# Kernel tuning notes

Hardware: AMD Instinct MI355X
Metric: run time of the kernel (lower is better)

The kernel has to match this reference:

```python
import jax, jax.numpy as jnp
import numpy as np

BSZ, MAX_LEN, INPUT_DIM = 4, 256, 1024
BIAFFINE, OUT, N_HEAD = 512, 512, 4
IN_HD = BIAFFINE // N_HEAD   # 128
OUT_HD = OUT // N_HEAD       # 128


def setup_inputs() -> dict:
    key = jax.random.key(0)
    ks = jax.random.split(key, 6)
    x = jax.random.normal(ks[0], (BSZ, MAX_LEN, INPUT_DIM), dtype=jnp.float32)
    # head/tail MLP linear params (dropout is identity at inference)
    scale_lin = 1.0 / np.sqrt(INPUT_DIM)
    Wh = jax.random.normal(ks[1], (BIAFFINE, INPUT_DIM), dtype=jnp.float32) * scale_lin
    bh = jnp.zeros((BIAFFINE,), dtype=jnp.float32)
    Wv = jax.random.normal(ks[2], (BIAFFINE, INPUT_DIM), dtype=jnp.float32) * scale_lin
    bv = jnp.zeros((BIAFFINE,), dtype=jnp.float32)
    # biaffine tensor, xavier_normal over last two dims fan
    xav = np.sqrt(2.0 / (IN_HD + IN_HD))
    W = jax.random.normal(ks[3], (N_HEAD, OUT_HD, IN_HD, IN_HD), dtype=jnp.float32) * xav
    return {"x": x, "Wh": Wh, "bh": bh, "Wv": Wv, "bv": bv, "W": W}


def reference(x, Wh, bh, Wv, bv, W):
    # head/tail MLPs: Linear + LeakyReLU (slope 0.01, torch default)
    h = jax.nn.leaky_relu(jnp.einsum('bld,od->blo', x, Wh) + bh)  # b l biaffine
    v = jax.nn.leaky_relu(jnp.einsum('bld,od->blo', x, Wv) + bv)
    bsz, max_len, _ = h.shape
    h = h.reshape(bsz, max_len, N_HEAD, IN_HD)
    v = v.reshape(bsz, max_len, N_HEAD, IN_HD)
    # 3-way biaffine contraction
    w = jnp.einsum('blhx,hdxy,bkhy->bhdlk', h, W, v)  # b h out_hd l k
    w = w.reshape(bsz, OUT, max_len, max_len)
    return jnp.transpose(w, (0, 2, 3, 1))  # b l k out
```

## Files before the change

kernel.cpp:

```cpp
#include <hip/hip_runtime.h>


typedef unsigned short u16;
typedef __attribute__((ext_vector_type(8))) short short8;
typedef __attribute__((ext_vector_type(4))) float f32x4;

__device__ __forceinline__ u16 f2bf(float f) {
  union { float f; unsigned u; } c; c.f = f;
  unsigned u = c.u;
  return (u16)((u + 0x7FFFu + ((u >> 16) & 1u)) >> 16);
}

__device__ __forceinline__ unsigned pack2(float a, float b) {
  return ((unsigned)f2bf(b) << 16) | (unsigned)f2bf(a);
}

__device__ __forceinline__ uint4 pack8(const float* __restrict__ g) {
  float4 f0 = *(const float4*)(g);
  float4 f1 = *(const float4*)(g + 4);
  uint4 o;
  o.x = pack2(f0.x, f0.y);
  o.y = pack2(f0.z, f0.w);
  o.z = pack2(f1.x, f1.y);
  o.w = pack2(f1.z, f1.w);
  return o;
}

__device__ __forceinline__ void tile_compute(const u16* As, const u16* Bs,
                                             f32x4 acc[4][4], int wm, int wn,
                                             int frow, int kq) {
  short8 af[4], bfr[4];
#pragma unroll
  for (int i = 0; i < 4; ++i)
    af[i] = *(const short8*)(As + (size_t)(wm + i * 16 + frow) * 32 + kq);
#pragma unroll
  for (int j = 0; j < 4; ++j)
    bfr[j] = *(const short8*)(Bs + (size_t)(wn + j * 16 + frow) * 32 + kq);
#pragma unroll
  for (int i = 0; i < 4; ++i)
#pragma unroll
    for (int j = 0; j < 4; ++j)
      acc[i][j] = __builtin_amdgcn_mfma_f32_16x16x32_bf16(af[i], bfr[j], acc[i][j], 0, 0, 0);
}

__device__ __forceinline__ void stage_bf16(const u16* __restrict__ ga,
                                           const u16* __restrict__ gb,
                                           u16* As, u16* Bs, int r, int seg) {
  uint4 a0 = *(const uint4*)ga;
  uint4 a1 = *(const uint4*)(ga + 8);
  uint4 b0 = *(const uint4*)gb;
  uint4 b1 = *(const uint4*)(gb + 8);
  __syncthreads();
  *(uint4*)(As + r * 32 + seg * 16) = a0;
  *(uint4*)(As + r * 32 + seg * 16 + 8) = a1;
  *(uint4*)(Bs + r * 32 + seg * 16) = b0;
  *(uint4*)(Bs + r * 32 + seg * 16 + 8) = b1;
  __syncthreads();
}

__global__ __launch_bounds__(256) void k0_twp(const float* __restrict__ W,
                                              u16* __restrict__ Wb) {
  __shared__ u16 t[128][129];
  int slice = blockIdx.x;
  const float* src = W + (size_t)slice * 16384;
  u16* dst = Wb + (size_t)slice * 16384;
  int tid = threadIdx.x;
  for (int e = tid; e < 16384; e += 256) {
    int xi = e >> 7, yi = e & 127;
    t[xi][yi] = f2bf(src[e]);
  }
  __syncthreads();
  for (int e = tid; e < 16384; e += 256) {
    int yi = e >> 7, xi = e & 127;
    dst[e] = t[xi][yi];
  }
}

__global__ __launch_bounds__(256) void k1_mlp(const float* __restrict__ x,
                                              const float* __restrict__ Wh,
                                              const float* __restrict__ bh,
                                              const float* __restrict__ Wv,
                                              const float* __restrict__ bv,
                                              u16* __restrict__ hmat,
                                              u16* __restrict__ vmat) {
  __shared__ __align__(16) u16 As[128 * 32];
  __shared__ __align__(16) u16 Bs[128 * 32];
  int tid = threadIdx.x;
  int m0 = blockIdx.y * 128;
  int n0 = blockIdx.x * 128;
  bool isV = (n0 >= 512);
  const float* Wsel = isV ? Wv : Wh;
  const float* bsel = isV ? bv : bh;
  int nW = isV ? (n0 - 512) : n0;
  int wave = tid >> 6, lane = tid & 63;
  int wm = (wave & 1) * 64, wn = (wave >> 1) * 64;
  int r = tid >> 1, seg = tid & 1;
  int frow = lane & 15, kq = (lane >> 4) * 8;
  f32x4 acc[4][4];
  f32x4 z = {0.f, 0.f, 0.f, 0.f};
#pragma unroll
  for (int i = 0; i < 4; ++i)
#pragma unroll
    for (int j = 0; j < 4; ++j) acc[i][j] = z;

  for (int k0 = 0; k0 < 1024; k0 += 32) {
    const float* ga = x + (size_t)(m0 + r) * 1024 + k0 + seg * 16;
    const float* gb = Wsel + (size_t)(nW + r) * 1024 + k0 + seg * 16;
    uint4 a0 = pack8(ga), a1 = pack8(ga + 8);
    uint4 b0 = pack8(gb), b1 = pack8(gb + 8);
    __syncthreads();
    *(uint4*)(As + r * 32 + seg * 16) = a0;
    *(uint4*)(As + r * 32 + seg * 16 + 8) = a1;
    *(uint4*)(Bs + r * 32 + seg * 16) = b0;
    *(uint4*)(Bs + r * 32 + seg * 16 + 8) = b1;
    __syncthreads();
    tile_compute(As, Bs, acc, wm, wn, frow, kq);
  }

  u16* dst = isV ? vmat : hmat;
#pragma unroll
  for (int i = 0; i < 4; ++i)
#pragma unroll
    for (int j = 0; j < 4; ++j)
#pragma unroll
      for (int rg = 0; rg < 4; ++rg) {
        int ml = wm + i * 16 + (lane >> 4) * 4 + rg;
        int nl = wn + j * 16 + (lane & 15);
        int mg = m0 + ml;
        int ng = n0 + nl;
        float val = acc[i][j][rg] + bsel[nW + nl];
        val = (val >= 0.f) ? val : 0.01f * val;
        int bb = mg >> 8, ll = mg & 255;
        int head = (ng & 511) >> 7, xcol = ng & 127;
        dst[(((size_t)(bb * 4 + head)) * 256 + ll) * 128 + xcol] = f2bf(val);
      }
}

__global__ __launch_bounds__(256) void k2_uw(const u16* __restrict__ hmat,
                                             const u16* __restrict__ Wb,
                                             u16* __restrict__ u, int b) {
  __shared__ __align__(16) u16 As[128 * 32];
  __shared__ __align__(16) u16 Bs[128 * 32];
  int tid = threadIdx.x;
  int h = blockIdx.z;
  int m0 = blockIdx.y * 128;
  int n0 = blockIdx.x * 128;
  const u16* A = hmat + ((size_t)(b * 4 + h) * 256 + m0) * 128;
  const u16* Bt = Wb + ((size_t)h * 16384 + n0) * 128;
  int wave = tid >> 6, lane = tid & 63;
  int wm = (wave & 1) * 64, wn = (wave >> 1) * 64;
  int r = tid >> 1, seg = tid & 1;
  int frow = lane & 15, kq = (lane >> 4) * 8;
  f32x4 acc[4][4];
  f32x4 z = {0.f, 0.f, 0.f, 0.f};
#pragma unroll
  for (int i = 0; i < 4; ++i)
#pragma unroll
    for (int j = 0; j < 4; ++j) acc[i][j] = z;

  for (int k0 = 0; k0 < 128; k0 += 32) {
    stage_bf16(A + (size_t)r * 128 + k0 + seg * 16,
               Bt + (size_t)r * 128 + k0 + seg * 16, As, Bs, r, seg);
    tile_compute(As, Bs, acc, wm, wn, frow, kq);
  }

  u16* C = u + ((size_t)h * 256 + m0) * 16384 + n0;
#pragma unroll
  for (int i = 0; i < 4; ++i)
#pragma unroll
    for (int j = 0; j < 4; ++j)
#pragma unroll
      for (int rg = 0; rg < 4; ++rg) {
        int ml = wm + i * 16 + (lane >> 4) * 4 + rg;
        int nl = wn + j * 16 + (lane & 15);
        C[(size_t)ml * 16384 + nl] = f2bf(acc[i][j][rg]);
      }
}

__global__ __launch_bounds__(256) void k3_out(const u16* __restrict__ vmat,
                                              const u16* __restrict__ u,
                                              float* __restrict__ out, int b) {
  __shared__ __align__(16) u16 As[128 * 32];
  __shared__ __align__(16) u16 Bs[128 * 32];
  int tid = threadIdx.x;
  int h = blockIdx.z;
  int l = blockIdx.y;
  int k0t = blockIdx.x * 128;
  const u16* A = vmat + ((size_t)(b * 4 + h) * 256 + k0t) * 128;
  const u16* Bt = u + ((size_t)h * 256 + l) * 16384;
  int wave = tid >> 6, lane = tid & 63;
  int wm = (wave & 1) * 64, wn = (wave >> 1) * 64;
  int r = tid >> 1, seg = tid & 1;
  int frow = lane & 15, kq = (lane >> 4) * 8;
  f32x4 acc[4][4];
  f32x4 z = {0.f, 0.f, 0.f, 0.f};
#pragma unroll
  for (int i = 0; i < 4; ++i)
#pragma unroll
    for (int j = 0; j < 4; ++j) acc[i][j] = z;

  for (int k0 = 0; k0 < 128; k0 += 32) {
    stage_bf16(A + (size_t)r * 128 + k0 + seg * 16,
               Bt + (size_t)r * 128 + k0 + seg * 16, As, Bs, r, seg);
    tile_compute(As, Bs, acc, wm, wn, frow, kq);
  }

#pragma unroll
  for (int i = 0; i < 4; ++i)
#pragma unroll
    for (int j = 0; j < 4; ++j)
#pragma unroll
      for (int rg = 0; rg < 4; ++rg) {
        int kk = k0t + wm + i * 16 + (lane >> 4) * 4 + rg;
        int d = wn + j * 16 + (lane & 15);
        out[(((size_t)b * 256 + l) * 256 + kk) * 512 + h * 128 + d] = acc[i][j][rg];
      }
}

extern "C" void kernel_launch(void* const* d_in, const int* in_sizes, int n_in,
                              void* d_out, int out_size, void* d_ws, size_t ws_size,
                              hipStream_t stream) {
  const float* x = (const float*)d_in[0];
  const float* Wh = (const float*)d_in[1];
  const float* bh = (const float*)d_in[2];
  const float* Wv = (const float*)d_in[3];
  const float* bv = (const float*)d_in[4];
  const float* W = (const float*)d_in[5];
  float* out = (float*)d_out;

  char* ws = (char*)d_ws;
  u16* Wb = (u16*)(ws);
  u16* hmat = (u16*)(ws + (16u << 20));
  u16* vmat = (u16*)(ws + (17u << 20));
  u16* u = (u16*)(ws + (18u << 20));

  hipLaunchKernelGGL(k0_twp, dim3(512), dim3(256), 0, stream, W, Wb);
  hipLaunchKernelGGL(k1_mlp, dim3(8, 8), dim3(256), 0, stream, x, Wh, bh, Wv, bv,
                     hmat, vmat);
  for (int b = 0; b < 4; ++b) {
    hipLaunchKernelGGL(k2_uw, dim3(128, 2, 4), dim3(256), 0, stream, hmat, Wb, u, b);
    hipLaunchKernelGGL(k3_out, dim3(2, 256, 4), dim3(256), 0, stream, vmat, u, out, b);
  }
}
```

Measured before the change: 718.7 us.

## Stage full-K tiles via direct global-to-LDS loads and batch all batches per launch

The per-K-step register-staged loop in k2/k3 is replaced by a single load of the whole 128x128 A and B tiles straight into LDS using global_load_lds, followed by one barrier and a full-K MFMA loop. The LDS layout becomes chunk-major (8-element columns) to suit the direct loads. When the workspace is large enough, the four per-batch launches collapse into one launch each for k2 and k3, with u sized for all batches. The k3 grid order also swaps so that l is the fastest-varying index. In exchange, LDS use grows to 64KB per block, which may lower occupancy, and the new tile layout may cause LDS bank conflicts.

```diff
diff --git a/kernel.cpp b/kernel.cpp
--- a/kernel.cpp
+++ b/kernel.cpp
@@ -4,6 +4,9 @@
 typedef unsigned short u16;
 typedef __attribute__((ext_vector_type(8))) short short8;
 typedef __attribute__((ext_vector_type(4))) float f32x4;
+
+typedef __attribute__((address_space(1))) const unsigned gu32;
+typedef __attribute__((address_space(3))) unsigned lu32;
 
 __device__ __forceinline__ u16 f2bf(float f) {
   union { float f; unsigned u; } c; c.f = f;
@@ -43,19 +46,37 @@
       acc[i][j] = __builtin_amdgcn_mfma_f32_16x16x32_bf16(af[i], bfr[j], acc[i][j], 0, 0, 0);
 }
 
-__device__ __forceinline__ void stage_bf16(const u16* __restrict__ ga,
-                                           const u16* __restrict__ gb,
-                                           u16* As, u16* Bs, int r, int seg) {
-  uint4 a0 = *(const uint4*)ga;
-  uint4 a1 = *(const uint4*)(ga + 8);
-  uint4 b0 = *(const uint4*)gb;
-  uint4 b1 = *(const uint4*)(gb + 8);
-  __syncthreads();
-  *(uint4*)(As + r * 32 + seg * 16) = a0;
-  *(uint4*)(As + r * 32 + seg * 16 + 8) = a1;
-  *(uint4*)(Bs + r * 32 + seg * 16) = b0;
-  *(uint4*)(Bs + r * 32 + seg * 16 + 8) = b1;
-  __syncthreads();
+__device__ __forceinline__ void stage_tile(const u16* __restrict__ g,
+                                           u16* lds, int wave, int lane) {
+#pragma unroll
+  for (int t = 0; t < 8; ++t) {
+    int qb = wave * 512 + t * 64;
+    int q = qb + lane;
+    const u16* src = g + (size_t)((q & 127) * 128 + (q >> 7) * 8);
+    __builtin_amdgcn_global_load_lds((gu32*)src, (lu32*)(lds + (size_t)qb * 8),
+                                     16, 0, 0);
+  }
+}
+
+__device__ __forceinline__ void compute_fullK(const u16* As, const u16* Bs,
+                                              f32x4 acc[4][4], int wm, int wn,
+                                              int frow, int chi) {
+#pragma unroll
+  for (int ks = 0; ks < 4; ++ks) {
+    int c = ks * 4 + chi;
+    short8 af[4], bfr[4];
+#pragma unroll
+    for (int i = 0; i < 4; ++i)
+      af[i] = *(const short8*)(As + ((size_t)c * 128 + wm + i * 16 + frow) * 8);
+#pragma unroll
+    for (int j = 0; j < 4; ++j)
+      bfr[j] = *(const short8*)(Bs + ((size_t)c * 128 + wn + j * 16 + frow) * 8);
+#pragma unroll
+    for (int i = 0; i < 4; ++i)
+#pragma unroll
+      for (int j = 0; j < 4; ++j)
+        acc[i][j] = __builtin_amdgcn_mfma_f32_16x16x32_bf16(af[i], bfr[j], acc[i][j], 0, 0, 0);
+  }
 }
 
 __global__ __launch_bounds__(256) void k0_twp(const float* __restrict__ W,
@@ -138,33 +159,32 @@
 
 __global__ __launch_bounds__(256) void k2_uw(const u16* __restrict__ hmat,
                                              const u16* __restrict__ Wb,
-                                             u16* __restrict__ u, int b) {
-  __shared__ __align__(16) u16 As[128 * 32];
-  __shared__ __align__(16) u16 Bs[128 * 32];
-  int tid = threadIdx.x;
-  int h = blockIdx.z;
+                                             u16* __restrict__ u, int b0) {
+  __shared__ __align__(16) u16 As[16384];
+  __shared__ __align__(16) u16 Bs[16384];
+  int tid = threadIdx.x, wave = tid >> 6, lane = tid & 63;
+  int z = blockIdx.z;
+  int b = b0 + (z >> 2), h = z & 3;
+  int n0 = blockIdx.x * 128;
   int m0 = blockIdx.y * 128;
-  int n0 = blockIdx.x * 128;
   const u16* A = hmat + ((size_t)(b * 4 + h) * 256 + m0) * 128;
   const u16* Bt = Wb + ((size_t)h * 16384 + n0) * 128;
-  int wave = tid >> 6, lane = tid & 63;
+  stage_tile(A, As, wave, lane);
+  stage_tile(Bt, Bs, wave, lane);
+
   int wm = (wave & 1) * 64, wn = (wave >> 1) * 64;
-  int r = tid >> 1, seg = tid & 1;
-  int frow = lane & 15, kq = (lane >> 4) * 8;
+  int frow = lane & 15, chi = lane >> 4;
   f32x4 acc[4][4];
-  f32x4 z = {0.f, 0.f, 0.f, 0.f};
-#pragma unroll
-  for (int i = 0; i < 4; ++i)
-#pragma unroll
-    for (int j = 0; j < 4; ++j) acc[i][j] = z;
-
-  for (int k0 = 0; k0 < 128; k0 += 32) {
-    stage_bf16(A + (size_t)r * 128 + k0 + seg * 16,
-               Bt + (size_t)r * 128 + k0 + seg * 16, As, Bs, r, seg);
-    tile_compute(As, Bs, acc, wm, wn, frow, kq);
-  }
-
-  u16* C = u + ((size_t)h * 256 + m0) * 16384 + n0;
+  f32x4 zz = {0.f, 0.f, 0.f, 0.f};
+#pragma unroll
+  for (int i = 0; i < 4; ++i)
+#pragma unroll
+    for (int j = 0; j < 4; ++j) acc[i][j] = zz;
+
+  __syncthreads();
+  compute_fullK(As, Bs, acc, wm, wn, frow, chi);
+
+  u16* C = u + ((size_t)z * 256 + m0) * 16384 + n0;
 #pragma unroll
   for (int i = 0; i < 4; ++i)
 #pragma unroll
@@ -179,31 +199,30 @@
 
 __global__ __launch_bounds__(256) void k3_out(const u16* __restrict__ vmat,
                                               const u16* __restrict__ u,
-                                              float* __restrict__ out, int b) {
-  __shared__ __align__(16) u16 As[128 * 32];
-  __shared__ __align__(16) u16 Bs[128 * 32];
-  int tid = threadIdx.x;
-  int h = blockIdx.z;
-  int l = blockIdx.y;
-  int k0t = blockIdx.x * 128;
+                                              float* __restrict__ out, int b0) {
+  __shared__ __align__(16) u16 As[16384];
+  __shared__ __align__(16) u16 Bs[16384];
+  int tid = threadIdx.x, wave = tid >> 6, lane = tid & 63;
+  int z = blockIdx.z;
+  int b = b0 + (z >> 2), h = z & 3;
+  int l = blockIdx.x;
+  int k0t = blockIdx.y * 128;
   const u16* A = vmat + ((size_t)(b * 4 + h) * 256 + k0t) * 128;
-  const u16* Bt = u + ((size_t)h * 256 + l) * 16384;
-  int wave = tid >> 6, lane = tid & 63;
+  const u16* Bt = u + ((size_t)z * 256 + l) * 16384;
+  stage_tile(A, As, wave, lane);
+  stage_tile(Bt, Bs, wave, lane);
+
   int wm = (wave & 1) * 64, wn = (wave >> 1) * 64;
-  int r = tid >> 1, seg = tid & 1;
-  int frow = lane & 15, kq = (lane >> 4) * 8;
+  int frow = lane & 15, chi = lane >> 4;
   f32x4 acc[4][4];
-  f32x4 z = {0.f, 0.f, 0.f, 0.f};
-#pragma unroll
-  for (int i = 0; i < 4; ++i)
-#pragma unroll
-    for (int j = 0; j < 4; ++j) acc[i][j] = z;
-
-  for (int k0 = 0; k0 < 128; k0 += 32) {
-    stage_bf16(A + (size_t)r * 128 + k0 + seg * 16,
-               Bt + (size_t)r * 128 + k0 + seg * 16, As, Bs, r, seg);
-    tile_compute(As, Bs, acc, wm, wn, frow, kq);
-  }
+  f32x4 zz = {0.f, 0.f, 0.f, 0.f};
+#pragma unroll
+  for (int i = 0; i < 4; ++i)
+#pragma unroll
+    for (int j = 0; j < 4; ++j) acc[i][j] = zz;
+
+  __syncthreads();
+  compute_fullK(As, Bs, acc, wm, wn, frow, chi);
 
 #pragma unroll
   for (int i = 0; i < 4; ++i)
@@ -237,8 +256,15 @@
   hipLaunchKernelGGL(k0_twp, dim3(512), dim3(256), 0, stream, W, Wb);
   hipLaunchKernelGGL(k1_mlp, dim3(8, 8), dim3(256), 0, stream, x, Wh, bh, Wv, bv,
                      hmat, vmat);
-  for (int b = 0; b < 4; ++b) {
-    hipLaunchKernelGGL(k2_uw, dim3(128, 2, 4), dim3(256), 0, stream, hmat, Wb, u, b);
-    hipLaunchKernelGGL(k3_out, dim3(2, 256, 4), dim3(256), 0, stream, vmat, u, out, b);
-  }
-}
+
+  size_t need = (18ull << 20) + (128ull << 20);
+  if (ws_size >= need) {
+    hipLaunchKernelGGL(k2_uw, dim3(128, 2, 16), dim3(256), 0, stream, hmat, Wb, u, 0);
+    hipLaunchKernelGGL(k3_out, dim3(256, 2, 16), dim3(256), 0, stream, vmat, u, out, 0);
+  } else {
+    for (int b = 0; b < 4; ++b) {
+      hipLaunchKernelGGL(k2_uw, dim3(128, 2, 4), dim3(256), 0, stream, hmat, Wb, u, b);
+      hipLaunchKernelGGL(k3_out, dim3(256, 2, 4), dim3(256), 0, stream, vmat, u, out, b);
+    }
+  }
+}
```

New measurement: 727.7 us. Within noise of the previous version (+1.2%).
